# Kernel tuning notes

Hardware: AMD Instinct MI355X
Metric: run time of the kernel (lower is better)

## Reference

```python
import jax, jax.numpy as jnp
import numpy as np

N = 100000   # nodes
E = 1600000  # edges
IN = 64      # in_channels
H = 64       # hidden_channels
OUT = 2      # out_channels
EPS = 1e-5   # BatchNorm eps


def setup_inputs() -> dict:
    key = jax.random.key(0)
    ks = jax.random.split(key, 14)
    x = jax.random.normal(ks[0], (N, IN), dtype=jnp.float32)
    edge_index = jax.random.randint(ks[1], (2, E), 0, N, dtype=jnp.int64)

    def lin(k, shape, fan_in):
        return (jax.random.normal(k, shape, dtype=jnp.float32) / np.float32(np.sqrt(fan_in)))

    return {
        "x": x,
        "edge_index": edge_index,
        "W0": lin(ks[2], (IN, H), IN),
        "b0": jnp.zeros((H,), jnp.float32),
        "g0": jnp.ones((H,), jnp.float32),
        "be0": jnp.zeros((H,), jnp.float32),
        "W1": lin(ks[3], (H, H), H),
        "b1": jnp.zeros((H,), jnp.float32),
        "g1": jnp.ones((H,), jnp.float32),
        "be1": jnp.zeros((H,), jnp.float32),
        "W2": lin(ks[4], (H, OUT), H),
        "b2": jnp.zeros((OUT,), jnp.float32),
    }


def _gcn_conv(h_in, W, b, src, dst, norm):
    # GCNConv: linear transform, then D^-1/2 (A + I) D^-1/2 aggregation, then bias
    h = h_in @ W                                   # [N, d_out]
    msg = h[src] * norm[:, None]                   # gather + scale, [E+N, d_out]
    agg = jax.ops.segment_sum(msg, dst, num_segments=N)
    return agg + b


def _batch_norm(h, gamma, beta):
    # training-mode BatchNorm1d over the node dimension (biased variance)
    mean = jnp.mean(h, axis=0)
    var = jnp.mean(jnp.square(h - mean), axis=0)
    return (h - mean) * jax.lax.rsqrt(var + EPS) * gamma + beta


def reference(x, edge_index, W0, b0, g0, be0, W1, b1, g1, be1, W2, b2):
    loop = jnp.arange(N, dtype=edge_index.dtype)
    src = jnp.concatenate([edge_index[0], loop])   # self loops appended
    dst = jnp.concatenate([edge_index[1], loop])
    deg = jax.ops.segment_sum(jnp.ones_like(dst, dtype=jnp.float32), dst, num_segments=N)
    dinv = jax.lax.rsqrt(deg)                      # deg >= 1 due to self loops
    norm = dinv[src] * dinv[dst]                   # [E+N]

    h = jax.nn.relu(_batch_norm(_gcn_conv(x, W0, b0, src, dst, norm), g0, be0))
    h_res = h
    h = jax.nn.relu(_batch_norm(_gcn_conv(h, W1, b1, src, dst, norm), g1, be1))
    h = h + h_res                                  # residual add
    out = _gcn_conv(h, W2, b2, src, dst, norm)     # [N, OUT]
    return out
```

## Files before the change

kernel.cpp:

```cpp
#include <hip/hip_runtime.h>


#define NN 100000
#define NE 1600000
#define NBUCK 1563
#define NBLK 256
#define CHUNK 6250
#define MAXB 2048

typedef unsigned short ushort_t;

__device__ __forceinline__ ushort_t f2bf(float f) {
    unsigned u = __float_as_uint(f);
    unsigned r = u + 0x7FFFu + ((u >> 16) & 1u);
    return (ushort_t)(r >> 16);
}
__device__ __forceinline__ float bf2f(ushort_t h) {
    return __uint_as_float(((unsigned)h) << 16);
}

__launch_bounds__(256)
__global__ void kA_hist(const int* __restrict__ dst, int* __restrict__ H) {
    __shared__ int h[NBUCK];
    int t = threadIdx.x, blk = blockIdx.x;
    for (int b = t; b < NBUCK; b += 256) h[b] = 0;
    __syncthreads();
    int e0 = blk * CHUNK;
    for (int e = e0 + t; e < e0 + CHUNK; e += 256) atomicAdd(&h[dst[e] >> 6], 1);
    __syncthreads();
    for (int b = t; b < NBUCK; b += 256) H[b * NBLK + blk] = h[b];
}
__launch_bounds__(256)
__global__ void kB1(const int* __restrict__ H, int* __restrict__ bsum) {
    __shared__ int sh[256];
    int b = blockIdx.x, t = threadIdx.x;
    sh[t] = H[b * NBLK + t];
    __syncthreads();
    for (int s = 128; s; s >>= 1) {
        if (t < s) sh[t] += sh[t + s];
        __syncthreads();
    }
    if (t == 0) bsum[b] = sh[0];
}
__global__ void kB2(const int* __restrict__ bsum, int* __restrict__ bbase) {
    __shared__ int sh[NBUCK];
    int t = threadIdx.x;
    for (int b = t; b < NBUCK; b += 256) sh[b] = bsum[b];
    __syncthreads();
    if (t == 0) {
        int acc = 0;
        for (int b = 0; b < NBUCK; ++b) { int v = sh[b]; sh[b] = acc; acc += v; }
        bbase[NBUCK] = acc;
    }
    __syncthreads();
    for (int b = t; b < NBUCK; b += 256) bbase[b] = sh[b];
}
__launch_bounds__(256)
__global__ void kB3(int* __restrict__ H, const int* __restrict__ bbase) {
    __shared__ int sh[256];
    int b = blockIdx.x, t = threadIdx.x;
    sh[t] = H[b * NBLK + t];
    __syncthreads();
    if (t == 0) {
        int acc = bbase[b];
        for (int i = 0; i < 256; ++i) { int v = sh[i]; sh[i] = acc; acc += v; }
    }
    __syncthreads();
    H[b * NBLK + t] = sh[t];
}
__launch_bounds__(256)
__global__ void kC_scatter(const int* __restrict__ src, const int* __restrict__ dst,
                           const int* __restrict__ O, unsigned int* __restrict__ sp) {
    __shared__ int cur[NBUCK];
    int t = threadIdx.x, blk = blockIdx.x;
    for (int b = t; b < NBUCK; b += 256) cur[b] = O[b * NBLK + blk];
    __syncthreads();
    int e0 = blk * CHUNK;
    for (int e = e0 + t; e < e0 + CHUNK; e += 256) {
        int d = dst[e], s = src[e];
        int p = atomicAdd(&cur[d >> 6], 1);
        sp[p] = ((unsigned int)(d & 63) << 24) | (unsigned int)s;
    }
}
__launch_bounds__(256)
__global__ void kD2_fin(const unsigned int* __restrict__ sp, const int* __restrict__ bbase,
                        int* __restrict__ csrc, int* __restrict__ rowstart,
                        int* __restrict__ cntg, float* __restrict__ dinv) {
    __shared__ int cnt[64], ofs[64], cur[64];
    __shared__ int tmp[MAXB];
    int b = blockIdx.x, t = threadIdx.x;
    int beg = bbase[b], end = bbase[b + 1], n = end - beg;
    if (t < 64) cnt[t] = 0;
    __syncthreads();
    for (int i = beg + t; i < end; i += 256) atomicAdd(&cnt[sp[i] >> 24], 1);
    __syncthreads();
    if (t == 0) {
        int acc = 0;
        for (int k = 0; k < 64; ++k) { int v = cnt[k]; ofs[k] = acc; cur[k] = acc; acc += v; }
    }
    __syncthreads();
    int node = b * 64 + t;
    if (t < 64 && node < NN) {
        rowstart[node] = beg + ofs[t];
        cntg[node] = cnt[t];
        dinv[node] = rsqrtf((float)(cnt[t] + 1));
    }
    if (n <= MAXB) {
        for (int i = beg + t; i < end; i += 256) {
            unsigned int v = sp[i];
            int p = atomicAdd(&cur[v >> 24], 1);
            tmp[p] = (int)(v & 0xFFFFFFu);
        }
        __syncthreads();
        for (int i = t; i < n; i += 256) csrc[beg + i] = tmp[i];
    } else {
        for (int i = beg + t; i < end; i += 256) {
            unsigned int v = sp[i];
            int p = atomicAdd(&cur[v >> 24], 1);
            csrc[beg + p] = (int)(v & 0xFFFFFFu);
        }
    }
}

template <int MODE>
__launch_bounds__(256, 4)
__global__ void k_gemm64(const float* __restrict__ X, const float* __restrict__ W,
                         const float* __restrict__ stats, const float* __restrict__ g,
                         const float* __restrict__ be, const float* __restrict__ dinv,
                         ushort_t* __restrict__ Yb, float* __restrict__ side) {
    __shared__ float xs[4][68];
    int t = threadIdx.x;
    int c = t & 63, rr = t >> 6;
    float w[64];
#pragma unroll
    for (int k = 0; k < 64; ++k) w[k] = W[k * 64 + c];
    float scale = 1.f, shift = 0.f;
    if (MODE == 1) {
        float mean = stats[c] * (1.0f / NN);
        float var = stats[64 + c] * (1.0f / NN) - mean * mean;
        scale = g[c] * rsqrtf(var + 1e-5f);
        shift = be[c] - mean * scale;
    }
    int base = blockIdx.x * 64;
#pragma unroll 2
    for (int rb = 0; rb < 16; ++rb) {
        int row = base + rb * 4 + rr;
        if (row >= NN) continue;
        float v = X[row * 64 + c];
        if (MODE == 1) {
            v = fmaxf(fmaf(v, scale, shift), 0.f);
            side[row * 64 + c] = v;
        }
        xs[rr][c] = v;
        const float4* xp = (const float4*)xs[rr];
        float a0 = 0.f, a1 = 0.f, a2 = 0.f, a3 = 0.f;
#pragma unroll
        for (int k4 = 0; k4 < 16; ++k4) {
            float4 xv = xp[k4];
            a0 = fmaf(xv.x, w[k4 * 4 + 0], a0);
            a1 = fmaf(xv.y, w[k4 * 4 + 1], a1);
            a2 = fmaf(xv.z, w[k4 * 4 + 2], a2);
            a3 = fmaf(xv.w, w[k4 * 4 + 3], a3);
        }
        Yb[row * 64 + c] = f2bf(dinv[row] * ((a0 + a1) + (a2 + a3)));
    }
}

__launch_bounds__(256)
__global__ void k_agg_csr(const ushort_t* __restrict__ Yb, const int* __restrict__ rowstart,
                          const int* __restrict__ cnt, const int* __restrict__ csrc,
                          const float* __restrict__ dinv, float* __restrict__ agg) {
    int wid = (blockIdx.x * blockDim.x + threadIdx.x) >> 6;
    int lane = threadIdx.x & 63;
    if (wid >= NN) return;
    int grp = lane >> 4;
    int l16 = lane & 15;
    int beg = rowstart[wid], n = cnt[wid];
    float4 acc = {0.f, 0.f, 0.f, 0.f};
    if (grp == 0) {
        ushort4 v = ((const ushort4*)(Yb + (long)wid * 64))[l16];
        acc.x = bf2f(v.x); acc.y = bf2f(v.y); acc.z = bf2f(v.z); acc.w = bf2f(v.w);
    }
    int j = grp;
    for (; j + 4 < n; j += 8) {
        int s0 = csrc[beg + j];
        int s1 = csrc[beg + j + 4];
        ushort4 v0 = ((const ushort4*)(Yb + (long)s0 * 64))[l16];
        ushort4 v1 = ((const ushort4*)(Yb + (long)s1 * 64))[l16];
        acc.x += bf2f(v0.x) + bf2f(v1.x);
        acc.y += bf2f(v0.y) + bf2f(v1.y);
        acc.z += bf2f(v0.z) + bf2f(v1.z);
        acc.w += bf2f(v0.w) + bf2f(v1.w);
    }
    if (j < n) {
        int s = csrc[beg + j];
        ushort4 v = ((const ushort4*)(Yb + (long)s * 64))[l16];
        acc.x += bf2f(v.x); acc.y += bf2f(v.y); acc.z += bf2f(v.z); acc.w += bf2f(v.w);
    }
#pragma unroll
    for (int m = 16; m <= 32; m <<= 1) {
        acc.x += __shfl_xor(acc.x, m);
        acc.y += __shfl_xor(acc.y, m);
        acc.z += __shfl_xor(acc.z, m);
        acc.w += __shfl_xor(acc.w, m);
    }
    if (grp == 0) {
        float d = dinv[wid];
        float4 r = {acc.x * d, acc.y * d, acc.z * d, acc.w * d};
        ((float4*)(agg + (long)wid * 64))[l16] = r;
    }
}

__launch_bounds__(256)
__global__ void k_bn_stats(const float* __restrict__ X, float* __restrict__ stats) {
    __shared__ float sh[512];
    int t = threadIdx.x;
    int c = t & 63, rr = t >> 6;
    float sum = 0.f, sq = 0.f;
    for (int r = blockIdx.x * 4 + rr; r < NN; r += gridDim.x * 4) {
        float v = X[r * 64 + c];
        sum += v;
        sq = fmaf(v, v, sq);
    }
    sh[t] = sum;
    sh[256 + t] = sq;
    __syncthreads();
    if (t < 64) {
        float s = sh[t] + sh[t + 64] + sh[t + 128] + sh[t + 192];
        float q = sh[256 + t] + sh[320 + t] + sh[384 + t] + sh[448 + t];
        atomicAdd(&stats[t], s);
        atomicAdd(&stats[64 + t], q);
    }
}

__launch_bounds__(256)
__global__ void k_gemm_out2(const float* __restrict__ X, const float* __restrict__ stats,
                            const float* __restrict__ g, const float* __restrict__ be,
                            const float* __restrict__ R, const float* __restrict__ W2,
                            const float* __restrict__ dinv, float* __restrict__ Tp) {
    int t = threadIdx.x;
    int lane = t & 63, wv = t >> 6;
    int row = blockIdx.x * 4 + wv;
    if (row >= NN) return;
    float mean = stats[lane] * (1.0f / NN);
    float var = stats[64 + lane] * (1.0f / NN) - mean * mean;
    float scale = g[lane] * rsqrtf(var + 1e-5f);
    float shift = be[lane] - mean * scale;
    float w0 = W2[lane * 2], w1 = W2[lane * 2 + 1];
    float v = X[row * 64 + lane];
    v = fmaxf(fmaf(v, scale, shift), 0.f) + R[row * 64 + lane];
    float p0 = v * w0, p1 = v * w1;
#pragma unroll
    for (int s = 32; s; s >>= 1) {
        p0 += __shfl_xor(p0, s);
        p1 += __shfl_xor(p1, s);
    }
    if (lane == 0) {
        float d = dinv[row];
        Tp[row * 2] = d * p0;
        Tp[row * 2 + 1] = d * p1;
    }
}

__launch_bounds__(256)
__global__ void k_out_csr(const float* __restrict__ Tp, const int* __restrict__ rowstart,
                          const int* __restrict__ cnt, const int* __restrict__ csrc,
                          const float* __restrict__ dinv, const float* __restrict__ b2,
                          float* __restrict__ out) {
    int id = blockIdx.x * blockDim.x + threadIdx.x;
    int node = id >> 3, l = id & 7;
    if (node >= NN) return;
    int beg = rowstart[node], n = cnt[node];
    float a0 = 0.f, a1 = 0.f;
    if (l == 0) { a0 = Tp[node * 2]; a1 = Tp[node * 2 + 1]; }
    for (int j = l; j < n; j += 8) {
        int s = csrc[beg + j];
        a0 += Tp[s * 2];
        a1 += Tp[s * 2 + 1];
    }
#pragma unroll
    for (int m = 1; m < 8; m <<= 1) {
        a0 += __shfl_xor(a0, m);
        a1 += __shfl_xor(a1, m);
    }
    if (l == 0) {
        float d = dinv[node];
        out[node * 2] = d * a0 + b2[0];
        out[node * 2 + 1] = d * a1 + b2[1];
    }
}

extern "C" void kernel_launch(void* const* d_in, const int* in_sizes, int n_in,
                              void* d_out, int out_size, void* d_ws, size_t ws_size,
                              hipStream_t stream) {
    const float* x   = (const float*)d_in[0];
    const int*   ei  = (const int*)d_in[1];
    const int*   src = ei;
    const int*   dst = ei + NE;
    const float* W0  = (const float*)d_in[2];
    const float* g0  = (const float*)d_in[4];
    const float* be0 = (const float*)d_in[5];
    const float* W1  = (const float*)d_in[6];
    const float* g1  = (const float*)d_in[8];
    const float* be1 = (const float*)d_in[9];
    const float* W2  = (const float*)d_in[10];
    const float* b2  = (const float*)d_in[11];
    float* out = (float*)d_out;

    int*   H      = (int*)d_ws;
    int*   bsum   = H + NBUCK * NBLK;
    int*   bbase  = bsum + 2048;
    unsigned int* sp = (unsigned int*)(bbase + 2048);
    int*   csrc   = (int*)(sp + NE);
    int*   rowstart = csrc + NE;
    int*   cntg   = rowstart + NN;
    float* dinv   = (float*)(cntg + NN);
    ushort_t* Ab  = (ushort_t*)(dinv + NN);
    float* B      = (float*)(Ab + NN * 64);
    float* C      = B + NN * 64;
    float* Tp     = C + NN * 64;
    float* stats0 = Tp + NN * 2;
    float* stats1 = stats0 + 128;

    hipMemsetAsync(stats0, 0, 256 * sizeof(float), stream);

    kA_hist<<<NBLK, 256, 0, stream>>>(dst, H);
    kB1<<<NBUCK, 256, 0, stream>>>(H, bsum);
    kB2<<<1, 256, 0, stream>>>(bsum, bbase);
    kB3<<<NBUCK, 256, 0, stream>>>(H, bbase);
    kC_scatter<<<NBLK, 256, 0, stream>>>(src, dst, H, sp);
    kD2_fin<<<NBUCK, 256, 0, stream>>>(sp, bbase, csrc, rowstart, cntg, dinv);

    int gemmGrid = (NN + 63) / 64;
    int aggGrid  = (NN * 64) / 256;

    k_gemm64<0><<<gemmGrid, 256, 0, stream>>>(x, W0, nullptr, nullptr, nullptr, dinv, Ab, nullptr);
    k_agg_csr<<<aggGrid, 256, 0, stream>>>(Ab, rowstart, cntg, csrc, dinv, B);
    k_bn_stats<<<256, 256, 0, stream>>>(B, stats0);

    k_gemm64<1><<<gemmGrid, 256, 0, stream>>>(B, W1, stats0, g0, be0, dinv, Ab, C);
    k_agg_csr<<<aggGrid, 256, 0, stream>>>(Ab, rowstart, cntg, csrc, dinv, B);
    k_bn_stats<<<256, 256, 0, stream>>>(B, stats1);

    k_gemm_out2<<<(NN + 3) / 4, 256, 0, stream>>>(B, stats1, g1, be1, C, W2, dinv, Tp);
    k_out_csr<<<(NN * 8 + 255) / 256, 256, 0, stream>>>(Tp, rowstart, cntg, csrc, dinv, b2, out);
}
```

Before: 419.9 us.

## Widen aggregation gathers to 16-byte loads and retune several pipeline kernels

```diff
diff --git a/kernel.cpp b/kernel.cpp
--- a/kernel.cpp
+++ b/kernel.cpp
@@ -15,20 +15,19 @@
     unsigned r = u + 0x7FFFu + ((u >> 16) & 1u);
     return (ushort_t)(r >> 16);
 }
-__device__ __forceinline__ float bf2f(ushort_t h) {
-    return __uint_as_float(((unsigned)h) << 16);
-}
-
-__launch_bounds__(256)
+__device__ __forceinline__ float bflo(unsigned u) { return __uint_as_float(u << 16); }
+__device__ __forceinline__ float bfhi(unsigned u) { return __uint_as_float(u & 0xFFFF0000u); }
+
+__launch_bounds__(1024)
 __global__ void kA_hist(const int* __restrict__ dst, int* __restrict__ H) {
     __shared__ int h[NBUCK];
     int t = threadIdx.x, blk = blockIdx.x;
-    for (int b = t; b < NBUCK; b += 256) h[b] = 0;
+    for (int b = t; b < NBUCK; b += 1024) h[b] = 0;
     __syncthreads();
     int e0 = blk * CHUNK;
-    for (int e = e0 + t; e < e0 + CHUNK; e += 256) atomicAdd(&h[dst[e] >> 6], 1);
-    __syncthreads();
-    for (int b = t; b < NBUCK; b += 256) H[b * NBLK + blk] = h[b];
+    for (int e = e0 + t; e < e0 + CHUNK; e += 1024) atomicAdd(&h[dst[e] >> 6], 1);
+    __syncthreads();
+    for (int b = t; b < NBUCK; b += 1024) H[b * NBLK + blk] = h[b];
 }
 __launch_bounds__(256)
 __global__ void kB1(const int* __restrict__ H, int* __restrict__ bsum) {
@@ -43,17 +42,31 @@
     if (t == 0) bsum[b] = sh[0];
 }
 __global__ void kB2(const int* __restrict__ bsum, int* __restrict__ bbase) {
-    __shared__ int sh[NBUCK];
+    __shared__ int part[256];
     int t = threadIdx.x;
-    for (int b = t; b < NBUCK; b += 256) sh[b] = bsum[b];
+    int loc[7];
+    int s = 0;
+#pragma unroll
+    for (int k = 0; k < 7; ++k) {
+        int i = t * 7 + k;
+        int v = (i < NBUCK) ? bsum[i] : 0;
+        loc[k] = s;
+        s += v;
+    }
+    part[t] = s;
     __syncthreads();
     if (t == 0) {
         int acc = 0;
-        for (int b = 0; b < NBUCK; ++b) { int v = sh[b]; sh[b] = acc; acc += v; }
+        for (int i = 0; i < 256; ++i) { int v = part[i]; part[i] = acc; acc += v; }
         bbase[NBUCK] = acc;
     }
     __syncthreads();
-    for (int b = t; b < NBUCK; b += 256) bbase[b] = sh[b];
+    int base = part[t];
+#pragma unroll
+    for (int k = 0; k < 7; ++k) {
+        int i = t * 7 + k;
+        if (i < NBUCK) bbase[i] = base + loc[k];
+    }
 }
 __launch_bounds__(256)
 __global__ void kB3(int* __restrict__ H, const int* __restrict__ bbase) {
@@ -166,6 +179,12 @@
     }
 }
 
+#define ACC8(q)                                                   \
+    acc0.x += bflo(q.x); acc0.y += bfhi(q.x);                     \
+    acc0.z += bflo(q.y); acc0.w += bfhi(q.y);                     \
+    acc1.x += bflo(q.z); acc1.y += bfhi(q.z);                     \
+    acc1.z += bflo(q.w); acc1.w += bfhi(q.w);
+
 __launch_bounds__(256)
 __global__ void k_agg_csr(const ushort_t* __restrict__ Yb, const int* __restrict__ rowstart,
                           const int* __restrict__ cnt, const int* __restrict__ csrc,
@@ -173,41 +192,45 @@
     int wid = (blockIdx.x * blockDim.x + threadIdx.x) >> 6;
     int lane = threadIdx.x & 63;
     if (wid >= NN) return;
-    int grp = lane >> 4;
-    int l16 = lane & 15;
+    int grp = lane >> 3;
+    int l8 = lane & 7;
     int beg = rowstart[wid], n = cnt[wid];
-    float4 acc = {0.f, 0.f, 0.f, 0.f};
+    float4 acc0 = {0.f, 0.f, 0.f, 0.f}, acc1 = {0.f, 0.f, 0.f, 0.f};
     if (grp == 0) {
-        ushort4 v = ((const ushort4*)(Yb + (long)wid * 64))[l16];
-        acc.x = bf2f(v.x); acc.y = bf2f(v.y); acc.z = bf2f(v.z); acc.w = bf2f(v.w);
+        uint4 q = ((const uint4*)(Yb + (long)wid * 64))[l8];
+        ACC8(q);
     }
     int j = grp;
-    for (; j + 4 < n; j += 8) {
+    for (; j + 8 < n; j += 16) {
         int s0 = csrc[beg + j];
-        int s1 = csrc[beg + j + 4];
-        ushort4 v0 = ((const ushort4*)(Yb + (long)s0 * 64))[l16];
-        ushort4 v1 = ((const ushort4*)(Yb + (long)s1 * 64))[l16];
-        acc.x += bf2f(v0.x) + bf2f(v1.x);
-        acc.y += bf2f(v0.y) + bf2f(v1.y);
-        acc.z += bf2f(v0.z) + bf2f(v1.z);
-        acc.w += bf2f(v0.w) + bf2f(v1.w);
+        int s1 = csrc[beg + j + 8];
+        uint4 q0 = ((const uint4*)(Yb + (long)s0 * 64))[l8];
+        uint4 q1 = ((const uint4*)(Yb + (long)s1 * 64))[l8];
+        ACC8(q0);
+        ACC8(q1);
     }
     if (j < n) {
         int s = csrc[beg + j];
-        ushort4 v = ((const ushort4*)(Yb + (long)s * 64))[l16];
-        acc.x += bf2f(v.x); acc.y += bf2f(v.y); acc.z += bf2f(v.z); acc.w += bf2f(v.w);
-    }
-#pragma unroll
-    for (int m = 16; m <= 32; m <<= 1) {
-        acc.x += __shfl_xor(acc.x, m);
-        acc.y += __shfl_xor(acc.y, m);
-        acc.z += __shfl_xor(acc.z, m);
-        acc.w += __shfl_xor(acc.w, m);
+        uint4 q = ((const uint4*)(Yb + (long)s * 64))[l8];
+        ACC8(q);
+    }
+#pragma unroll
+    for (int m = 8; m <= 32; m <<= 1) {
+        acc0.x += __shfl_xor(acc0.x, m);
+        acc0.y += __shfl_xor(acc0.y, m);
+        acc0.z += __shfl_xor(acc0.z, m);
+        acc0.w += __shfl_xor(acc0.w, m);
+        acc1.x += __shfl_xor(acc1.x, m);
+        acc1.y += __shfl_xor(acc1.y, m);
+        acc1.z += __shfl_xor(acc1.z, m);
+        acc1.w += __shfl_xor(acc1.w, m);
     }
     if (grp == 0) {
         float d = dinv[wid];
-        float4 r = {acc.x * d, acc.y * d, acc.z * d, acc.w * d};
-        ((float4*)(agg + (long)wid * 64))[l16] = r;
+        float4 r0 = {acc0.x * d, acc0.y * d, acc0.z * d, acc0.w * d};
+        float4 r1 = {acc1.x * d, acc1.y * d, acc1.z * d, acc1.w * d};
+        ((float4*)(agg + (long)wid * 64))[l8 * 2] = r0;
+        ((float4*)(agg + (long)wid * 64))[l8 * 2 + 1] = r1;
     }
 }
 
@@ -324,7 +347,7 @@
 
     hipMemsetAsync(stats0, 0, 256 * sizeof(float), stream);
 
-    kA_hist<<<NBLK, 256, 0, stream>>>(dst, H);
+    kA_hist<<<NBLK, 1024, 0, stream>>>(dst, H);
     kB1<<<NBUCK, 256, 0, stream>>>(H, bsum);
     kB2<<<1, 256, 0, stream>>>(bsum, bbase);
     kB3<<<NBUCK, 256, 0, stream>>>(H, bbase);
@@ -336,11 +359,11 @@
 
     k_gemm64<0><<<gemmGrid, 256, 0, stream>>>(x, W0, nullptr, nullptr, nullptr, dinv, Ab, nullptr);
     k_agg_csr<<<aggGrid, 256, 0, stream>>>(Ab, rowstart, cntg, csrc, dinv, B);
-    k_bn_stats<<<256, 256, 0, stream>>>(B, stats0);
+    k_bn_stats<<<1024, 256, 0, stream>>>(B, stats0);
 
     k_gemm64<1><<<gemmGrid, 256, 0, stream>>>(B, W1, stats0, g0, be0, dinv, Ab, C);
     k_agg_csr<<<aggGrid, 256, 0, stream>>>(Ab, rowstart, cntg, csrc, dinv, B);
-    k_bn_stats<<<256, 256, 0, stream>>>(B, stats1);
+    k_bn_stats<<<1024, 256, 0, stream>>>(B, stats1);
 
     k_gemm_out2<<<(NN + 3) / 4, 256, 0, stream>>>(B, stats1, g1, be1, C, W2, dinv, Tp);
     k_out_csr<<<(NN * 8 + 255) / 256, 256, 0, stream>>>(Tp, rowstart, cntg, csrc, dinv, b2, out);
```

New measurement: 376.4 us. 10.3% less time.
